# Kernel optimization log

Hardware: AMD Instinct MI355X
Metric: run time of the kernel (lower is better)

The kernel has to match this reference:

```python
import jax, jax.numpy as jnp
import numpy as np

MAX_DEPTH = 6
NUM_TREES = 64
LEAF_DIMS = 128
D_IN = 512
BATCH = 4096
N_INTERNAL = 2 ** MAX_DEPTH - 1  # 63
N_LEAVES = 2 ** MAX_DEPTH        # 64


def setup_inputs() -> dict:
    key = jax.random.key(0)
    ks = jax.random.split(key, 4)
    x = jax.random.normal(ks[0], (BATCH, D_IN), dtype=jnp.float32)
    # Stacked internal-node dense layers, node i at index i (level order, node_index ordering)
    W = jax.random.normal(ks[1], (N_INTERNAL, D_IN, NUM_TREES), dtype=jnp.float32) / np.sqrt(D_IN)
    b = jnp.zeros((N_INTERNAL, NUM_TREES), dtype=jnp.float32)
    leaf_weight = jax.random.normal(ks[2], (N_LEAVES, LEAF_DIMS, NUM_TREES), dtype=jnp.float32)
    gates = jax.random.normal(ks[3], (N_LEAVES, LEAF_DIMS, NUM_TREES), dtype=jnp.float32)
    return {"x": x, "W": W, "b": b, "leaf_weight": leaf_weight, "gates": gates}


def reference(x, W, b, leaf_weight, gates):
    # All internal-node gating probabilities in one batched matmul:
    # g[b, n, t] = sigmoid(x[b] @ W[n] + b[n])  for every internal node n, tree t
    g = jax.nn.sigmoid(jnp.einsum('bd,ndt->bnt', x, W) + b[None, :, :])  # [B, 63, T]

    B = x.shape[0]
    T = W.shape[-1]
    # Path probability to each leaf, built level by level.
    # Level l has 2^l nodes at internal indices [2^l - 1, 2^(l+1) - 2];
    # interleaving (left=p*g, right=p*(1-g)) matches node_index child ordering.
    p = jnp.ones((B, 1, T), dtype=x.dtype)
    for level in range(MAX_DEPTH):
        start = 2 ** level - 1
        n_lvl = 2 ** level
        gl = g[:, start:start + n_lvl, :]                  # [B, n_lvl, T]
        children = jnp.stack([p * gl, p * (1.0 - gl)], axis=2)  # [B, n_lvl, 2, T]
        p = children.reshape(B, 2 * n_lvl, T)
    # p: [B, n_leaves, T] leaf path probabilities

    # Softmax mixture-of-experts gate over trees, then weighted leaf mixture:
    # out[b, d] = sum_{l, t} p[b, l, t] * leaf_weight[l, d, t] * softmax(gates, -1)[l, d, t]
    w = leaf_weight * jax.nn.softmax(gates, axis=-1)  # [L, D, T]
    out = jnp.einsum('blt,ldt->bd', p, w)
    return out
```

## Files before the change

### kernel.cpp

```cpp
#include <hip/hip_runtime.h>
#include <stdint.h>

#define BATCH 4096
#define DIN   512
#define NT    64
#define NL    64
#define LD    128

typedef __attribute__((ext_vector_type(8))) short bf16x8;
typedef __attribute__((ext_vector_type(8))) _Float16 f16x8;
typedef __attribute__((ext_vector_type(4))) float f32x4;

typedef const __attribute__((address_space(1))) unsigned char* gcp_t;
typedef __attribute__((address_space(3))) unsigned char* lp_t;

__device__ __forceinline__ void gl_lds16(const void* g, void* l) {
  __builtin_amdgcn_global_load_lds((gcp_t)g, (lp_t)l, 16, 0, 0);
}

__device__ __forceinline__ unsigned pk_bf16(float a, float b) {
  union { float f; unsigned u; } ua, ub;
  ua.f = a; ub.f = b;
  return __builtin_amdgcn_perm(ub.u + 0x8000u, ua.u + 0x8000u, 0x07060302u);
}

__global__ __launch_bounds__(256) void prep_all_k(
    const float* __restrict__ x, const float* __restrict__ W,
    const float* __restrict__ gates, const float* __restrict__ lw,
    unsigned short* __restrict__ xb, unsigned short* __restrict__ Wt,
    unsigned short* __restrict__ Wv2, float* __restrict__ out) {
  __shared__ float smem[12288];
  const int bx = blockIdx.x;
  const int tid = threadIdx.x;

  if (bx < 2048) {
    int i = bx * 256 + tid;
    float4 v = ((const float4*)x)[i];
    uint2 o;
    o.x = pk_bf16(v.x, v.y);
    o.y = pk_bf16(v.z, v.w);
    ((uint2*)xb)[i] = o;
  } else if (bx < 2304) {
    int bb = bx - 2048;
    int n = bb >> 2, d0 = (bb & 3) * 128;
    float* buf = smem;
    if (n < 63) {
      for (int it = 0; it < 32; ++it) {
        int idx = it * 256 + tid;
        buf[idx] = W[n * 32768 + (d0 + (idx >> 6)) * 64 + (idx & 63)];
      }
    }
    __syncthreads();
    int t = tid >> 2, q = tid & 3;
    unsigned vals[16];
    #pragma unroll
    for (int j = 0; j < 16; ++j) {
      float va = (n < 63) ? buf[(q * 32 + 2 * j) * 64 + t] : 0.0f;
      float vb = (n < 63) ? buf[(q * 32 + 2 * j + 1) * 64 + t] : 0.0f;
      vals[j] = (n < 63) ? pk_bf16(va, vb) : 0u;
    }
    uint4* dst = (uint4*)(Wt + t * 32768 + n * 512 + d0 + q * 32);
    const uint4* src = (const uint4*)vals;
    dst[0] = src[0]; dst[1] = src[1]; dst[2] = src[2]; dst[3] = src[3];
  } else if (bx < 2432) {
    int d = bx - 2304;
    float* gb = smem;
    float* lb = smem + 4096;
    float* wv = smem + 8192;
    for (int it = 0; it < 16; ++it) {
      int idx = it * 256 + tid;
      int l = idx >> 6;
      int ga = l * 8192 + d * 64 + (idx & 63);
      gb[idx] = gates[ga];
      lb[idx] = lw[ga];
    }
    __syncthreads();
    int wave = tid >> 6, lane = tid & 63;
    for (int l = wave; l < 64; l += 4) {
      float v = gb[l * 64 + lane];
      float mx = v;
      for (int m = 32; m >= 1; m >>= 1) mx = fmaxf(mx, __shfl_xor(mx, m));
      float e = __expf(v - mx);
      float s = e;
      for (int m = 32; m >= 1; m >>= 1) s += __shfl_xor(s, m);
      wv[l * 64 + lane] = lb[l * 64 + lane] * e / s;
    }
    __syncthreads();
    #pragma unroll
    for (int c = 0; c < 2; ++c) {
      int k0 = tid * 16 + c * 8;
      unsigned o[4];
      #pragma unroll
      for (int j = 0; j < 4; ++j) {
        int ka = k0 + 2 * j, kb = k0 + 2 * j + 1;
        o[j] = pk_bf16(wv[(ka & 63) * 64 + (ka >> 6)], wv[(kb & 63) * 64 + (kb >> 6)]);
      }
      *(uint4*)(Wv2 + (long)d * 4096 + k0) = *(const uint4*)o;
    }
  } else {
    float4 z = {0.f, 0.f, 0.f, 0.f};
    int base = (bx - 2432) * 256 + tid;
    float4* o4 = (float4*)out;
    #pragma unroll
    for (int k = 0; k < 16; ++k)
      o4[k * 8192 + base] = z;
  }
}

__global__ __launch_bounds__(512, 4) void gemm1_tree_k(
    const unsigned short* __restrict__ xb,
    const unsigned short* __restrict__ Wt,
    const float* __restrict__ bias,
    unsigned short* __restrict__ P)
{
  __shared__ __align__(16) char smem[73728];
  unsigned short* AsB = (unsigned short*)smem;
  unsigned short* BsB = (unsigned short*)(smem + 49152);
  _Float16* gbuf = (_Float16*)smem;

  const int tid = threadIdx.x;
  const int wave = tid >> 6, lane = tid & 63;

  const int lin = blockIdx.x;
  const int rr = lin & 7, kq = lin >> 3;
  const int b0 = ((kq & 3) | ((rr & 3) << 2)) * 256;
  const int t0 = ((kq >> 2) | ((rr >> 2) << 4)) * 2;

  const int wm = (wave >> 1) * 64, wn = (wave & 1) * 64;
  const int mrow = lane & 15, kg = lane >> 4;
  const int slot = (kg ^ ((mrow >> 1) & 3)) * 8;

  float bv[4];
  #pragma unroll
  for (int j = 0; j < 4; ++j) {
    int n = j * 16 + mrow;
    bv[j] = (n < 63) ? bias[n * 64 + t0 + (wave & 1)] : 0.0f;
  }

  const f32x4 zero = {0.f, 0.f, 0.f, 0.f};
  f32x4 acc[4][4];
  #pragma unroll
  for (int i = 0; i < 4; ++i)
    #pragma unroll
    for (int j = 0; j < 4; ++j) acc[i][j] = zero;

  const int g0 = tid;
  const int g1 = tid + 512;
  const int c0 = ((g0 & 3) ^ ((g0 >> 3) & 3)) * 8;
  const int c1 = ((g1 & 3) ^ ((g1 >> 3) & 3)) * 8;
  const unsigned short* Ag0 = xb + (long)(b0 + (g0 >> 2)) * 512 + c0;
  const unsigned short* Ag1 = xb + (long)(b0 + (g1 >> 2)) * 512 + c1;
  const unsigned short* Bg0 = Wt + (long)(t0 * 64 + (g0 >> 2)) * 512 + c0;
  const int lofsA0 = wave * 512;
  const int lofsA1 = wave * 512 + 4096;
  const int lofsB  = wave * 512;

  gl_lds16(Ag0, AsB + lofsA0);
  gl_lds16(Ag1, AsB + lofsA1);
  gl_lds16(Bg0, BsB + lofsB);
  gl_lds16(Ag0 + 32, AsB + 8192 + lofsA0);
  gl_lds16(Ag1 + 32, AsB + 8192 + lofsA1);
  gl_lds16(Bg0 + 32, BsB + 4096 + lofsB);

  for (int it = 0; it < 16; ++it) {
    const int bufA = (it % 3) * 8192;
    const int bufB = (it % 3) * 4096;
    if (it < 15) {
      asm volatile("s_waitcnt vmcnt(3) lgkmcnt(0)" ::: "memory");
    } else {
      asm volatile("s_waitcnt vmcnt(0) lgkmcnt(0)" ::: "memory");
    }
    asm volatile("s_barrier" ::: "memory");

    if (it < 14) {
      const int kk = (it + 2) * 32;
      const int nA = ((it + 2) % 3) * 8192;
      const int nB = ((it + 2) % 3) * 4096;
      gl_lds16(Ag0 + kk, AsB + nA + lofsA0);
      gl_lds16(Ag1 + kk, AsB + nA + lofsA1);
      gl_lds16(Bg0 + kk, BsB + nB + lofsB);
    }

    bf16x8 fa[4], fb[4];
    #pragma unroll
    for (int i = 0; i < 4; ++i)
      fa[i] = *(const bf16x8*)(AsB + bufA + (wm + i * 16 + mrow) * 32 + slot);
    #pragma unroll
    for (int j = 0; j < 4; ++j)
      fb[j] = *(const bf16x8*)(BsB + bufB + (wn + j * 16 + mrow) * 32 + slot);
    #pragma unroll
    for (int i = 0; i < 4; ++i)
      #pragma unroll
      for (int j = 0; j < 4; ++j)
        acc[i][j] = __builtin_amdgcn_mfma_f32_16x16x32_bf16(fa[i], fb[j], acc[i][j], 0, 0, 0);
  }

  __syncthreads();

  #pragma unroll
  for (int i = 0; i < 4; ++i)
    #pragma unroll
    for (int j = 0; j < 4; ++j) {
      int col = wn + j * 16 + mrow;
      int oct = col >> 3, sub = col & 7;
      #pragma unroll
      for (int r = 0; r < 4; ++r) {
        int row = wm + i * 16 + kg * 4 + r;
        float z = acc[i][j][r] + bv[j];
        gbuf[row * 128 + ((oct ^ (row & 15)) << 3) + sub] =
            (_Float16)__builtin_amdgcn_rcpf(1.0f + __expf(-z));
      }
    }
  __syncthreads();

  {
    const int row = tid >> 1, tr = tid & 1;
    const _Float16* grow = gbuf + row * 128;
    const int rx = row & 15;
    float g[63];
    #pragma unroll
    for (int c = 0; c < 8; ++c) {
      f16x8 gv = *(const f16x8*)(grow + (((tr * 8 + c) ^ rx) << 3));
      #pragma unroll
      for (int j = 0; j < 8; ++j) {
        int n = c * 8 + j;
        if (n < 63) g[n] = (float)gv[j];
      }
    }
    float P3[8];
    {
      float a0 = g[0],            a1 = 1.0f - g[0];
      float c0_ = a0 * g[1],      c1_ = a0 * (1.0f - g[1]);
      float c2_ = a1 * g[2],      c3_ = a1 * (1.0f - g[2]);
      P3[0] = c0_ * g[3];  P3[1] = c0_ * (1.0f - g[3]);
      P3[2] = c1_ * g[4];  P3[3] = c1_ * (1.0f - g[4]);
      P3[4] = c2_ * g[5];  P3[5] = c2_ * (1.0f - g[5]);
      P3[6] = c3_ * g[6];  P3[7] = c3_ * (1.0f - g[6]);
    }
    unsigned short* prow = P + (long)(b0 + row) * 4096 + (t0 + tr) * 64;
    #pragma unroll
    for (int o = 0; o < 8; ++o) {
      float g3 = g[7 + o];
      float q0 = P3[o] * g3, q1 = P3[o] * (1.0f - g3);
      float g4a = g[15 + 2 * o], g4b = g[16 + 2 * o];
      float r0 = q0 * g4a, r1 = q0 * (1.0f - g4a);
      float r2 = q1 * g4b, r3 = q1 * (1.0f - g4b);
      unsigned ou[4];
      #pragma unroll
      for (int h = 0; h < 4; ++h) {
        float g5 = g[31 + 4 * o + h];
        float rr2 = (h == 0) ? r0 : (h == 1) ? r1 : (h == 2) ? r2 : r3;
        ou[h] = pk_bf16(rr2 * g5, rr2 * (1.0f - g5));
      }
      *(uint4*)(prow + o * 8) = *(const uint4*)ou;
    }
  }
}

__global__ __launch_bounds__(256, 4) void gemm2_k(
    const unsigned short* __restrict__ P,
    const unsigned short* __restrict__ Wv2,
    float* __restrict__ out)
{
  __shared__ unsigned short AsB[2][64 * 32];
  __shared__ unsigned short BsB[2][128 * 32];
  const int tid = threadIdx.x;
  const int wave = tid >> 6, lane = tid & 63;
  const int b0 = blockIdx.x * 64;
  const int k0 = blockIdx.y * 1024;

  const f32x4 zero = {0.f, 0.f, 0.f, 0.f};
  f32x4 acc[2][4];
  #pragma unroll
  for (int i = 0; i < 2; ++i)
    #pragma unroll
    for (int j = 0; j < 4; ++j) acc[i][j] = zero;

  const int g0 = wave * 64 + lane;
  const int g1 = g0 + 256;
  const int c0 = ((g0 & 3) ^ ((g0 >> 3) & 3)) * 8;
  const int c1 = ((g1 & 3) ^ ((g1 >> 3) & 3)) * 8;
  const unsigned short* Ag0 = P + (long)(b0 + (g0 >> 2)) * 4096 + k0 + c0;
  const unsigned short* Bg0 = Wv2 + (long)(g0 >> 2) * 4096 + k0 + c0;
  const unsigned short* Bg1 = Wv2 + (long)(g1 >> 2) * 4096 + k0 + c1;
  const int lofs = wave * 512;

  const int wm = (wave >> 1) * 32, wn = (wave & 1) * 64;
  const int mrow = lane & 15, kg = lane >> 4;
  const int slot = (kg ^ ((mrow >> 1) & 3)) * 8;

  gl_lds16(Ag0, AsB[0] + lofs);
  gl_lds16(Bg0, BsB[0] + lofs);
  gl_lds16(Bg1, BsB[0] + lofs + 2048);

  for (int it = 0; it < 32; ++it) {
    const int buf = it & 1;
    if (it < 31) {
      const int kk = (it + 1) * 32;
      const int nbuf = (it + 1) & 1;
      gl_lds16(Ag0 + kk, AsB[nbuf] + lofs);
      gl_lds16(Bg0 + kk, BsB[nbuf] + lofs);
      gl_lds16(Bg1 + kk, BsB[nbuf] + lofs + 2048);
      asm volatile("s_waitcnt vmcnt(3)" ::: "memory");
    } else {
      asm volatile("s_waitcnt vmcnt(0)" ::: "memory");
    }
    asm volatile("s_barrier" ::: "memory");

    bf16x8 fa[2], fb[4];
    #pragma unroll
    for (int i = 0; i < 2; ++i)
      fa[i] = *(const bf16x8*)(AsB[buf] + (wm + i * 16 + mrow) * 32 + slot);
    #pragma unroll
    for (int j = 0; j < 4; ++j)
      fb[j] = *(const bf16x8*)(BsB[buf] + (wn + j * 16 + mrow) * 32 + slot);
    #pragma unroll
    for (int i = 0; i < 2; ++i)
      #pragma unroll
      for (int j = 0; j < 4; ++j)
        acc[i][j] = __builtin_amdgcn_mfma_f32_16x16x32_bf16(fa[i], fb[j], acc[i][j], 0, 0, 0);

    asm volatile("s_waitcnt lgkmcnt(0)" ::: "memory");
    asm volatile("s_barrier" ::: "memory");
  }

  #pragma unroll
  for (int i = 0; i < 2; ++i)
    #pragma unroll
    for (int j = 0; j < 4; ++j) {
      int col = wn + j * 16 + mrow;
      #pragma unroll
      for (int r = 0; r < 4; ++r) {
        int row = wm + i * 16 + kg * 4 + r;
        atomicAdd(&out[(long)(b0 + row) * 128 + col], acc[i][j][r]);
      }
    }
}

extern "C" void kernel_launch(void* const* d_in, const int* in_sizes, int n_in,
                              void* d_out, int out_size, void* d_ws, size_t ws_size,
                              hipStream_t stream) {
  const float* x     = (const float*)d_in[0];
  const float* W     = (const float*)d_in[1];
  const float* b     = (const float*)d_in[2];
  const float* lw    = (const float*)d_in[3];
  const float* gates = (const float*)d_in[4];
  float* out = (float*)d_out;

  char* ws = (char*)d_ws;
  unsigned short* xb  = (unsigned short*)(ws);
  unsigned short* Wt  = (unsigned short*)(ws + (4l  << 20));
  unsigned short* Wv2 = (unsigned short*)(ws + (8l  << 20));
  unsigned short* P   = (unsigned short*)(ws + (16l << 20));

  hipLaunchKernelGGL(prep_all_k,   dim3(2464), dim3(256), 0, stream,
                     x, W, gates, lw, xb, Wt, Wv2, out);
  hipLaunchKernelGGL(gemm1_tree_k, dim3(512),  dim3(512), 0, stream, xb, Wt, b, P);
  hipLaunchKernelGGL(gemm2_k,      dim3(64, 4), dim3(256), 0, stream, P, Wv2, out);
}
```

Measured before the change: 134.7 us.

## Enlarge gemm1 tile to 256x256 with split-phase pipelined MFMA schedule

The first GEMM's block tile grows from 256 batch rows by 128 columns (2 trees) to 256 by 256 (4 trees). This halves the grid to 256 blocks and raises LDS to 128 KB with a new XOR swizzle. The K loop is split into two phases that interleave LDS fragment reads, async global-to-LDS loads and MFMA bursts under s_setprio, with barriers between phases. The aim is more operand reuse per loaded byte and better overlap of loads with matrix math. The cost is lower occupancy (2 blocks per CU), twice the accumulator registers, and only 256 blocks to fill the CUs.

```diff
diff --git a/kernel.cpp b/kernel.cpp
--- a/kernel.cpp
+++ b/kernel.cpp
@@ -107,152 +107,188 @@
   }
 }
 
-__global__ __launch_bounds__(512, 4) void gemm1_tree_k(
+__global__ __launch_bounds__(512, 2) void gemm1_tree_k(
     const unsigned short* __restrict__ xb,
     const unsigned short* __restrict__ Wt,
     const float* __restrict__ bias,
     unsigned short* __restrict__ P)
 {
-  __shared__ __align__(16) char smem[73728];
-  unsigned short* AsB = (unsigned short*)smem;
-  unsigned short* BsB = (unsigned short*)(smem + 49152);
+  __shared__ __align__(16) char smem[131072];
+  unsigned short* lds = (unsigned short*)smem;
   _Float16* gbuf = (_Float16*)smem;
 
   const int tid = threadIdx.x;
   const int wave = tid >> 6, lane = tid & 63;
 
-  const int lin = blockIdx.x;
-  const int rr = lin & 7, kq = lin >> 3;
-  const int b0 = ((kq & 3) | ((rr & 3) << 2)) * 256;
-  const int t0 = ((kq >> 2) | ((rr >> 2) << 4)) * 2;
-
-  const int wm = (wave >> 1) * 64, wn = (wave & 1) * 64;
+  const int bid = blockIdx.x;
+  const int xcd = bid & 7, idx = bid >> 3;
+  const int bm = ((xcd >> 1) << 2) | (idx >> 3);
+  const int bn = ((xcd & 1) << 3) | (idx & 7);
+  const int b0  = bm << 8;
+  const int n0  = bn << 8;
+  const int t0g = bn << 2;
+
+  const int wm = (wave >> 2) << 7;
+  const int wn = (wave & 3) << 6;
   const int mrow = lane & 15, kg = lane >> 4;
-  const int slot = (kg ^ ((mrow >> 1) & 3)) * 8;
+
+  const int r2b   = tid >> 3;
+  const int inner = (tid & 7) ^ (r2b & 7);
+  const int grow0 = (r2b << 1) + (inner >> 2);
+  const int gcol  = (inner & 3) << 3;
+  const unsigned short* SA0 = xb + (long)(b0 + grow0) * 512 + gcol;
+  const unsigned short* SA1 = xb + (long)(b0 + grow0 + 128) * 512 + gcol;
+  const unsigned short* SB0 = Wt + (long)(n0 + grow0) * 512 + gcol;
+  const unsigned short* SB1 = Wt + (long)(n0 + grow0 + 128) * 512 + gcol;
+  const int ldst0 = tid * 8;
+  const int ldst1 = tid * 8 + 4096;
+
+  const int rsl  = ((((mrow & 1) << 2) | kg) ^ ((mrow >> 1) & 7)) << 3;
+  const int ar2  = (wm >> 1) + (mrow >> 1);
+  const int br2  = (wn >> 1) + (mrow >> 1);
 
   float bv[4];
   #pragma unroll
   for (int j = 0; j < 4; ++j) {
-    int n = j * 16 + mrow;
-    bv[j] = (n < 63) ? bias[n * 64 + t0 + (wave & 1)] : 0.0f;
+    int node = j * 16 + mrow;
+    bv[j] = (node < 63) ? bias[node * 64 + t0g + (wave & 3)] : 0.0f;
   }
 
   const f32x4 zero = {0.f, 0.f, 0.f, 0.f};
-  f32x4 acc[4][4];
-  #pragma unroll
-  for (int i = 0; i < 4; ++i)
+  f32x4 acc[8][4];
+  #pragma unroll
+  for (int i = 0; i < 8; ++i)
     #pragma unroll
     for (int j = 0; j < 4; ++j) acc[i][j] = zero;
 
-  const int g0 = tid;
-  const int g1 = tid + 512;
-  const int c0 = ((g0 & 3) ^ ((g0 >> 3) & 3)) * 8;
-  const int c1 = ((g1 & 3) ^ ((g1 >> 3) & 3)) * 8;
-  const unsigned short* Ag0 = xb + (long)(b0 + (g0 >> 2)) * 512 + c0;
-  const unsigned short* Ag1 = xb + (long)(b0 + (g1 >> 2)) * 512 + c1;
-  const unsigned short* Bg0 = Wt + (long)(t0 * 64 + (g0 >> 2)) * 512 + c0;
-  const int lofsA0 = wave * 512;
-  const int lofsA1 = wave * 512 + 4096;
-  const int lofsB  = wave * 512;
-
-  gl_lds16(Ag0, AsB + lofsA0);
-  gl_lds16(Ag1, AsB + lofsA1);
-  gl_lds16(Bg0, BsB + lofsB);
-  gl_lds16(Ag0 + 32, AsB + 8192 + lofsA0);
-  gl_lds16(Ag1 + 32, AsB + 8192 + lofsA1);
-  gl_lds16(Bg0 + 32, BsB + 4096 + lofsB);
-
-  for (int it = 0; it < 16; ++it) {
-    const int bufA = (it % 3) * 8192;
-    const int bufB = (it % 3) * 4096;
-    if (it < 15) {
-      asm volatile("s_waitcnt vmcnt(3) lgkmcnt(0)" ::: "memory");
-    } else {
-      asm volatile("s_waitcnt vmcnt(0) lgkmcnt(0)" ::: "memory");
+  gl_lds16(SA0,      lds + 0     + ldst0);
+  gl_lds16(SA1,      lds + 0     + ldst1);
+  gl_lds16(SB0,      lds + 24576 + ldst0);
+  gl_lds16(SB1,      lds + 24576 + ldst1);
+  gl_lds16(SA0 + 32, lds + 8192  + ldst0);
+  gl_lds16(SA1 + 32, lds + 8192  + ldst1);
+  gl_lds16(SB0 + 32, lds + 24576 + 8192 + ldst0);
+  gl_lds16(SB1 + 32, lds + 24576 + 8192 + ldst1);
+  asm volatile("s_waitcnt vmcnt(4)" ::: "memory");
+  asm volatile("s_barrier" ::: "memory");
+
+  for (int t = 0; t < 16; ++t) {
+    const int ab = (t % 3) * 8192;
+    const int bb = 24576 + (t % 3) * 8192;
+    const int sbuf = ((t + 2) % 3) * 8192;
+    const int kofs = (t + 2) * 32;
+
+    bf16x8 fa[4], fb[4];
+    #pragma unroll
+    for (int m = 0; m < 4; ++m)
+      fa[m] = *(const bf16x8*)(lds + ab + (ar2 + m * 8) * 64 + rsl);
+    #pragma unroll
+    for (int j = 0; j < 4; ++j)
+      fb[j] = *(const bf16x8*)(lds + bb + (br2 + j * 8) * 64 + rsl);
+    if (t < 14) {
+      gl_lds16(SA0 + kofs, lds + sbuf + ldst0);
+      gl_lds16(SA1 + kofs, lds + sbuf + ldst1);
     }
     asm volatile("s_barrier" ::: "memory");
-
-    if (it < 14) {
-      const int kk = (it + 2) * 32;
-      const int nA = ((it + 2) % 3) * 8192;
-      const int nB = ((it + 2) % 3) * 4096;
-      gl_lds16(Ag0 + kk, AsB + nA + lofsA0);
-      gl_lds16(Ag1 + kk, AsB + nA + lofsA1);
-      gl_lds16(Bg0 + kk, BsB + nB + lofsB);
-    }
-
-    bf16x8 fa[4], fb[4];
-    #pragma unroll
-    for (int i = 0; i < 4; ++i)
-      fa[i] = *(const bf16x8*)(AsB + bufA + (wm + i * 16 + mrow) * 32 + slot);
-    #pragma unroll
-    for (int j = 0; j < 4; ++j)
-      fb[j] = *(const bf16x8*)(BsB + bufB + (wn + j * 16 + mrow) * 32 + slot);
-    #pragma unroll
-    for (int i = 0; i < 4; ++i)
+    asm volatile("s_waitcnt lgkmcnt(0)" ::: "memory");
+    __builtin_amdgcn_s_setprio(1);
+    #pragma unroll
+    for (int m = 0; m < 4; ++m)
       #pragma unroll
       for (int j = 0; j < 4; ++j)
-        acc[i][j] = __builtin_amdgcn_mfma_f32_16x16x32_bf16(fa[i], fb[j], acc[i][j], 0, 0, 0);
+        acc[m][j] = __builtin_amdgcn_mfma_f32_16x16x32_bf16(fa[m], fb[j], acc[m][j], 0, 0, 0);
+    __builtin_amdgcn_s_setprio(0);
+
+    bf16x8 fa2[4];
+    #pragma unroll
+    for (int m = 0; m < 4; ++m)
+      fa2[m] = *(const bf16x8*)(lds + ab + (ar2 + 32 + m * 8) * 64 + rsl);
+    if (t < 14) {
+      gl_lds16(SB0 + kofs, lds + 24576 + sbuf + ldst0);
+      gl_lds16(SB1 + kofs, lds + 24576 + sbuf + ldst1);
+    }
+    asm volatile("s_barrier" ::: "memory");
+    asm volatile("s_waitcnt lgkmcnt(0)" ::: "memory");
+    __builtin_amdgcn_s_setprio(1);
+    #pragma unroll
+    for (int m = 0; m < 4; ++m)
+      #pragma unroll
+      for (int j = 0; j < 4; ++j)
+        acc[4 + m][j] = __builtin_amdgcn_mfma_f32_16x16x32_bf16(fa2[m], fb[j], acc[4 + m][j], 0, 0, 0);
+    __builtin_amdgcn_s_setprio(0);
+
+    if (t < 15) {
+      if (t <= 13) {
+        asm volatile("s_waitcnt vmcnt(4)" ::: "memory");
+      } else {
+        asm volatile("s_waitcnt vmcnt(0)" ::: "memory");
+      }
+      asm volatile("s_barrier" ::: "memory");
+    }
   }
 
   __syncthreads();
 
   #pragma unroll
-  for (int i = 0; i < 4; ++i)
+  for (int ai = 0; ai < 8; ++ai)
     #pragma unroll
     for (int j = 0; j < 4; ++j) {
       int col = wn + j * 16 + mrow;
-      int oct = col >> 3, sub = col & 7;
+      int ch = col >> 3, sub = col & 7;
       #pragma unroll
       for (int r = 0; r < 4; ++r) {
-        int row = wm + i * 16 + kg * 4 + r;
-        float z = acc[i][j][r] + bv[j];
-        gbuf[row * 128 + ((oct ^ (row & 15)) << 3) + sub] =
+        int row = wm + ai * 16 + kg * 4 + r;
+        float z = acc[ai][j][r] + bv[j];
+        gbuf[row * 256 + (((ch ^ (row & 31)) << 3) | sub)] =
             (_Float16)__builtin_amdgcn_rcpf(1.0f + __expf(-z));
       }
     }
   __syncthreads();
 
   {
-    const int row = tid >> 1, tr = tid & 1;
-    const _Float16* grow = gbuf + row * 128;
-    const int rx = row & 15;
-    float g[63];
-    #pragma unroll
-    for (int c = 0; c < 8; ++c) {
-      f16x8 gv = *(const f16x8*)(grow + (((tr * 8 + c) ^ rx) << 3));
-      #pragma unroll
-      for (int j = 0; j < 8; ++j) {
-        int n = c * 8 + j;
-        if (n < 63) g[n] = (float)gv[j];
-      }
-    }
-    float P3[8];
-    {
-      float a0 = g[0],            a1 = 1.0f - g[0];
-      float c0_ = a0 * g[1],      c1_ = a0 * (1.0f - g[1]);
-      float c2_ = a1 * g[2],      c3_ = a1 * (1.0f - g[2]);
-      P3[0] = c0_ * g[3];  P3[1] = c0_ * (1.0f - g[3]);
-      P3[2] = c1_ * g[4];  P3[3] = c1_ * (1.0f - g[4]);
-      P3[4] = c2_ * g[5];  P3[5] = c2_ * (1.0f - g[5]);
-      P3[6] = c3_ * g[6];  P3[7] = c3_ * (1.0f - g[6]);
-    }
-    unsigned short* prow = P + (long)(b0 + row) * 4096 + (t0 + tr) * 64;
-    #pragma unroll
-    for (int o = 0; o < 8; ++o) {
-      float g3 = g[7 + o];
-      float q0 = P3[o] * g3, q1 = P3[o] * (1.0f - g3);
-      float g4a = g[15 + 2 * o], g4b = g[16 + 2 * o];
-      float r0 = q0 * g4a, r1 = q0 * (1.0f - g4a);
-      float r2 = q1 * g4b, r3 = q1 * (1.0f - g4b);
-      unsigned ou[4];
-      #pragma unroll
-      for (int h = 0; h < 4; ++h) {
-        float g5 = g[31 + 4 * o + h];
-        float rr2 = (h == 0) ? r0 : (h == 1) ? r1 : (h == 2) ? r2 : r3;
-        ou[h] = pk_bf16(rr2 * g5, rr2 * (1.0f - g5));
-      }
-      *(uint4*)(prow + o * 8) = *(const uint4*)ou;
+    const int row = tid >> 1;
+    const int rx = row & 31;
+    #pragma unroll
+    for (int k2 = 0; k2 < 2; ++k2) {
+      const int tree = (tid & 1) + 2 * k2;
+      float g[63];
+      #pragma unroll
+      for (int c = 0; c < 8; ++c) {
+        int ch = tree * 8 + c;
+        f16x8 gv = *(const f16x8*)(gbuf + row * 256 + ((ch ^ rx) << 3));
+        #pragma unroll
+        for (int j = 0; j < 8; ++j) {
+          int n = c * 8 + j;
+          if (n < 63) g[n] = (float)gv[j];
+        }
+      }
+      float P3[8];
+      {
+        float a0 = g[0],            a1 = 1.0f - g[0];
+        float c0_ = a0 * g[1],      c1_ = a0 * (1.0f - g[1]);
+        float c2_ = a1 * g[2],      c3_ = a1 * (1.0f - g[2]);
+        P3[0] = c0_ * g[3];  P3[1] = c0_ * (1.0f - g[3]);
+        P3[2] = c1_ * g[4];  P3[3] = c1_ * (1.0f - g[4]);
+        P3[4] = c2_ * g[5];  P3[5] = c2_ * (1.0f - g[5]);
+        P3[6] = c3_ * g[6];  P3[7] = c3_ * (1.0f - g[6]);
+      }
+      unsigned short* prow = P + (long)(b0 + row) * 4096 + (t0g + tree) * 64;
+      #pragma unroll
+      for (int o = 0; o < 8; ++o) {
+        float g3 = g[7 + o];
+        float q0 = P3[o] * g3, q1 = P3[o] * (1.0f - g3);
+        float g4a = g[15 + 2 * o], g4b = g[16 + 2 * o];
+        float r0 = q0 * g4a, r1 = q0 * (1.0f - g4a);
+        float r2 = q1 * g4b, r3 = q1 * (1.0f - g4b);
+        unsigned ou[4];
+        #pragma unroll
+        for (int h = 0; h < 4; ++h) {
+          float g5 = g[31 + 4 * o + h];
+          float rr2 = (h == 0) ? r0 : (h == 1) ? r1 : (h == 2) ? r2 : r3;
+          ou[h] = pk_bf16(rr2 * g5, rr2 * (1.0f - g5));
+        }
+        *(uint4*)(prow + o * 8) = *(const uint4*)ou;
+      }
     }
   }
 }
@@ -355,6 +391,6 @@
 
   hipLaunchKernelGGL(prep_all_k,   dim3(2464), dim3(256), 0, stream,
                      x, W, gates, lw, xb, Wt, Wv2, out);
-  hipLaunchKernelGGL(gemm1_tree_k, dim3(512),  dim3(512), 0, stream, xb, Wt, b, P);
+  hipLaunchKernelGGL(gemm1_tree_k, dim3(256),  dim3(512), 0, stream, xb, Wt, b, P);
   hipLaunchKernelGGL(gemm2_k,      dim3(64, 4), dim3(256), 0, stream, P, Wv2, out);
 }
```

New measurement: 139.4 us. 1.04x slower.
